# Optimization experiments

Measured on AMD Instinct MI355X. Metric: run time of the kernel, lower is better.

Reference implementation:

```python
import jax, jax.numpy as jnp
import numpy as np

B = 64            # number of graphs
NPG = 64          # nodes per graph (static; lengths are all equal here)
N = B * NPG       # total nodes = sum(lengths)
LT = 128          # max text tokens per node
LL = 32           # max labels per node
VOCAB = 50000
TOTAL_NUM = 100000
D = 256           # embedding_text == embedding_label == hidden_dimension
OUT = 1024


def setup_inputs() -> dict:
    key = jax.random.key(0)
    ks = jax.random.split(key, 12)
    return {
        "text_ids": jax.random.randint(ks[0], (N, LT), 0, VOCAB),
        "label_ids": jax.random.randint(ks[1], (N, LL), 0, TOTAL_NUM),
        "text_len": jax.random.randint(ks[2], (N,), 1, LT + 1),
        "label_len": jax.random.randint(ks[3], (N,), 1, LL + 1),
        "word_emb": jax.random.normal(ks[4], (VOCAB, D), jnp.float32) * 0.02,
        "label_emb": jax.random.normal(ks[5], (TOTAL_NUM, D), jnp.float32) * 0.02,
        "Wg_text": jax.random.normal(ks[6], (D, D), jnp.float32) * (1.0 / np.sqrt(D)),
        "Wg_label": jax.random.normal(ks[7], (D, D), jnp.float32) * (1.0 / np.sqrt(D)),
        "w_adap": jax.random.normal(ks[8], (2,), jnp.float32),
        "W1": jax.random.normal(ks[9], (D, D), jnp.float32) * (1.0 / np.sqrt(D)),
        "b1": jnp.zeros((D,), jnp.float32),
        "Wout": jax.random.normal(ks[10], (D, OUT), jnp.float32) * (1.0 / np.sqrt(D)),
        "bout": jnp.zeros((OUT,), jnp.float32),
    }


def _ragged_bag(table, ids, lens, mean):
    # gather rows then masked sum over the ragged axis (EmbeddingBag-style)
    L = ids.shape[1]
    mask = (jnp.arange(L)[None, :] < lens[:, None]).astype(table.dtype)  # [N, L]
    emb = table[ids]                                                     # [N, L, D]
    out = jnp.einsum("nld,nl->nd", emb, mask)
    if mean:
        out = out / lens[:, None].astype(table.dtype)
    return out


def reference(text_ids, label_ids, text_len, label_len, word_emb, label_emb,
              Wg_text, Wg_label, w_adap, W1, b1, Wout, bout):
    # fetchFeature: per-node ragged mean of word embeddings, ragged sum of label embeddings
    text_out = _ragged_bag(word_emb, text_ids, text_len, mean=True)    # [N, D]
    label_out = _ragged_bag(label_emb, label_ids, label_len, mean=False)  # [N, D]

    # weighted_GCN surrogate: per-type linear projection + relu, then per-graph mean readout
    h_t = jax.nn.relu(text_out @ Wg_text)   # [N, D]
    h_l = jax.nn.relu(label_out @ Wg_label)  # [N, D]
    seg = jnp.repeat(jnp.arange(B), NPG)     # graph id per node
    r_t = jax.ops.segment_sum(h_t, seg, num_segments=B) / NPG  # [B, D]
    r_l = jax.ops.segment_sum(h_l, seg, num_segments=B) / NPG  # [B, D]

    # adap: Linear(2,1,bias=False) over stacked (text,label), then MLLinear fusion
    fused = jnp.stack([r_t, r_l], axis=-1) @ w_adap  # [B, D]
    h = jax.nn.relu(fused @ W1 + b1)
    return h @ Wout + bout  # [B, OUT]
```

## Files before the change

### kernel.cpp

```cpp
#include <hip/hip_runtime.h>

#define NN      4096
#define BG      64
#define NPG_    64
#define LT_     128
#define LL_     32
#define D_      256
#define OUT_    1024

typedef __attribute__((ext_vector_type(8))) short bf16x8;
typedef __attribute__((ext_vector_type(4))) float f32x4;

__device__ __forceinline__ void split_bf16(float v, unsigned short& hi, unsigned short& lo) {
    union { float f; unsigned u; } a; a.f = v;
    const unsigned hu = (a.u + 0x8000u) & 0xFFFF0000u;
    union { unsigned u; float f; } h; h.u = hu;
    const float r = v - h.f;
    union { float f; unsigned u; } b; b.f = r;
    hi = (unsigned short)(hu >> 16);
    lo = (unsigned short)(((b.u + 0x8000u) & 0xFFFF0000u) >> 16);
}

__global__ __launch_bounds__(256) void convw_kernel(
    const float* __restrict__ Wg_text,
    const float* __restrict__ Wg_label,
    unsigned short* __restrict__ Wpk)
{
    const int b   = blockIdx.x;
    const int mat = b >> 7;
    const int nt  = (b >> 3) & 15;
    const int ks  = b & 7;
    const float* __restrict__ W = mat ? Wg_label : Wg_text;
    const int tid = threadIdx.x;

    #pragma unroll
    for (int r = 0; r < 2; ++r) {
        const int idx = tid + 256 * r;
        const int kl  = idx >> 4;
        const int c16 = idx & 15;
        const int k   = ks * 32 + kl;
        const float v = W[(size_t)k * D_ + nt * 16 + c16];
        unsigned short h, l;
        split_bf16(v, h, l);
        const int lane = c16 + 16 * ((kl >> 3) & 3);
        const int e    = kl & 7;
        const size_t bh = ((((size_t)mat * 2 + 0) * 16 + nt) * 8 + ks) * 512 + lane * 8 + e;
        const size_t bl = ((((size_t)mat * 2 + 1) * 16 + nt) * 8 + ks) * 512 + lane * 8 + e;
        Wpk[bh] = h;
        Wpk[bl] = l;
    }
}

__global__ __launch_bounds__(256) void gather_kernel(
    const int*   __restrict__ text_ids,
    const int*   __restrict__ label_ids,
    const int*   __restrict__ text_len,
    const int*   __restrict__ label_len,
    const float* __restrict__ word_emb,
    const float* __restrict__ label_emb,
    unsigned short* __restrict__ xh_t,
    unsigned short* __restrict__ xl_t,
    unsigned short* __restrict__ xh_l,
    unsigned short* __restrict__ xl_l)
{
    __shared__ int   sIds[LT_ + LL_];
    __shared__ float redT[4][D_];
    __shared__ float redL[4][D_];

    const int n    = blockIdx.x;
    const int tid  = threadIdx.x;
    const int wave = tid >> 6;
    const int lane = tid & 63;

    if (tid < LT_)               sIds[tid] = text_ids [(size_t)n * LT_ + tid];
    else if (tid < LT_ + LL_)    sIds[tid] = label_ids[(size_t)n * LL_ + (tid - LT_)];
    const int lt = text_len[n];
    const int ll = label_len[n];
    __syncthreads();

    float4 aT = make_float4(0.f, 0.f, 0.f, 0.f);
    float4 aL = make_float4(0.f, 0.f, 0.f, 0.f);

    {
        const float* __restrict__ bp = word_emb + (size_t)lane * 4;
        #pragma unroll 8
        for (int l = wave; l < lt; l += 4) {
            const float4 v = *reinterpret_cast<const float4*>(bp + (size_t)sIds[l] * D_);
            aT.x += v.x; aT.y += v.y; aT.z += v.z; aT.w += v.w;
        }
    }
    {
        const float* __restrict__ bp = label_emb + (size_t)lane * 4;
        #pragma unroll 8
        for (int l = wave; l < ll; l += 4) {
            const float4 v = *reinterpret_cast<const float4*>(bp + (size_t)sIds[LT_ + l] * D_);
            aL.x += v.x; aL.y += v.y; aL.z += v.z; aL.w += v.w;
        }
    }

    *reinterpret_cast<float4*>(&redT[wave][lane * 4]) = aT;
    *reinterpret_cast<float4*>(&redL[wave][lane * 4]) = aL;
    __syncthreads();

    const float t  = ((redT[0][tid] + redT[1][tid]) + (redT[2][tid] + redT[3][tid])) / (float)lt;
    const float lv =  (redL[0][tid] + redL[1][tid]) + (redL[2][tid] + redL[3][tid]);

    unsigned short h, l;
    const size_t o = (size_t)n * D_ + tid;
    split_bf16(t,  h, l);  xh_t[o] = h;  xl_t[o] = l;
    split_bf16(lv, h, l);  xh_l[o] = h;  xl_l[o] = l;
}

__global__ __launch_bounds__(512, 4) void proj_kernel(
    const unsigned short* __restrict__ xh_t,
    const unsigned short* __restrict__ xl_t,
    const unsigned short* __restrict__ xh_l,
    const unsigned short* __restrict__ xl_l,
    const unsigned short* __restrict__ Wpk,
    const float* __restrict__ w_adap,
    float*       __restrict__ h_comb)
{
    __shared__ __align__(16) short ldsX[4][16 * D_];

    const int tid   = threadIdx.x;
    const int wave  = tid >> 6;
    const int lane  = tid & 63;
    const int ntile = blockIdx.x >> 1;
    const int chalf = blockIdx.x & 1;
    const int base  = ntile * 16;

    {
        const int nd = tid >> 5, ch = tid & 31;
        const size_t g = (size_t)(base + nd) * D_ + ch * 8;
        const int d = nd * D_ + ((ch ^ (nd & 7)) * 8);
        *reinterpret_cast<int4*>(&ldsX[0][d]) = *reinterpret_cast<const int4*>(&xh_t[g]);
        *reinterpret_cast<int4*>(&ldsX[1][d]) = *reinterpret_cast<const int4*>(&xl_t[g]);
        *reinterpret_cast<int4*>(&ldsX[2][d]) = *reinterpret_cast<const int4*>(&xh_l[g]);
        *reinterpret_cast<int4*>(&ldsX[3][d]) = *reinterpret_cast<const int4*>(&xl_l[g]);
    }
    __syncthreads();

    const int nt  = chalf * 8 + wave;
    const int row = lane & 15;
    const int kc  = lane >> 4;
    f32x4 accT = {0.f, 0.f, 0.f, 0.f};
    f32x4 accL = {0.f, 0.f, 0.f, 0.f};

    #pragma unroll
    for (int ks = 0; ks < 8; ++ks) {
        const int aidx = row * D_ + (((ks * 4 + kc) ^ (row & 7)) * 8);
        const bf16x8 ath  = *reinterpret_cast<const bf16x8*>(&ldsX[0][aidx]);
        const bf16x8 atl  = *reinterpret_cast<const bf16x8*>(&ldsX[1][aidx]);
        const bf16x8 alh  = *reinterpret_cast<const bf16x8*>(&ldsX[2][aidx]);
        const bf16x8 all_ = *reinterpret_cast<const bf16x8*>(&ldsX[3][aidx]);

        const bf16x8 bth = *reinterpret_cast<const bf16x8*>(
            &Wpk[(((size_t)0 * 16 + nt) * 8 + ks) * 512 + lane * 8]);
        const bf16x8 btl = *reinterpret_cast<const bf16x8*>(
            &Wpk[(((size_t)1 * 16 + nt) * 8 + ks) * 512 + lane * 8]);
        const bf16x8 blh = *reinterpret_cast<const bf16x8*>(
            &Wpk[(((size_t)2 * 16 + nt) * 8 + ks) * 512 + lane * 8]);
        const bf16x8 bll = *reinterpret_cast<const bf16x8*>(
            &Wpk[(((size_t)3 * 16 + nt) * 8 + ks) * 512 + lane * 8]);

        accT = __builtin_amdgcn_mfma_f32_16x16x32_bf16(ath, bth, accT, 0, 0, 0);
        accT = __builtin_amdgcn_mfma_f32_16x16x32_bf16(ath, btl, accT, 0, 0, 0);
        accT = __builtin_amdgcn_mfma_f32_16x16x32_bf16(atl, bth, accT, 0, 0, 0);

        accL = __builtin_amdgcn_mfma_f32_16x16x32_bf16(alh, blh, accL, 0, 0, 0);
        accL = __builtin_amdgcn_mfma_f32_16x16x32_bf16(alh, bll, accL, 0, 0, 0);
        accL = __builtin_amdgcn_mfma_f32_16x16x32_bf16(all_, blh, accL, 0, 0, 0);
    }

    const float w0r = w_adap[0] * (1.0f / (float)NPG_);
    const float w1r = w_adap[1] * (1.0f / (float)NPG_);
    #pragma unroll
    for (int r = 0; r < 4; ++r) {
        const int node = base + kc * 4 + r;
        const int col  = nt * 16 + row;
        const float ht = accT[r] > 0.f ? accT[r] : 0.f;
        const float hl = accL[r] > 0.f ? accL[r] : 0.f;
        h_comb[(size_t)node * D_ + col] = w0r * ht + w1r * hl;
    }
}

__global__ __launch_bounds__(256) void graph_kernel(
    const float* __restrict__ h_comb,
    const float* __restrict__ W1,
    const float* __restrict__ b1,
    const float* __restrict__ Wout,
    const float* __restrict__ bout,
    float*       __restrict__ out)
{
    __shared__ float fused[D_];
    __shared__ float hrow[D_];

    const int bx   = blockIdx.x;
    const int b    = bx >> 2;
    const int part = bx & 3;
    const int tid  = threadIdx.x;

    float acc = 0.f;
    const float* __restrict__ basep = h_comb + (size_t)b * NPG_ * D_ + tid;
    #pragma unroll 8
    for (int n = 0; n < NPG_; ++n) acc += basep[(size_t)n * D_];
    fused[tid] = acc;
    __syncthreads();

    float a1 = b1[tid];
    for (int d = 0; d < D_; ++d)
        a1 = fmaf(fused[d], W1[(size_t)d * D_ + tid], a1);
    hrow[tid] = a1 > 0.f ? a1 : 0.f;
    __syncthreads();

    const int j = part * 256 + tid;
    float o = bout[j];
    for (int d = 0; d < D_; ++d)
        o = fmaf(hrow[d], Wout[(size_t)d * OUT_ + j], o);
    out[(size_t)b * OUT_ + j] = o;
}

extern "C" void kernel_launch(void* const* d_in, const int* in_sizes, int n_in,
                              void* d_out, int out_size, void* d_ws, size_t ws_size,
                              hipStream_t stream) {
    const int*   text_ids  = (const int*)  d_in[0];
    const int*   label_ids = (const int*)  d_in[1];
    const int*   text_len  = (const int*)  d_in[2];
    const int*   label_len = (const int*)  d_in[3];
    const float* word_emb  = (const float*)d_in[4];
    const float* label_emb = (const float*)d_in[5];
    const float* Wg_text   = (const float*)d_in[6];
    const float* Wg_label  = (const float*)d_in[7];
    const float* w_adap    = (const float*)d_in[8];
    const float* W1        = (const float*)d_in[9];
    const float* b1        = (const float*)d_in[10];
    const float* Wout      = (const float*)d_in[11];
    const float* bout      = (const float*)d_in[12];

    char* ws = (char*)d_ws;
    float*          h_comb = (float*)ws;
    unsigned short* xh_t   = (unsigned short*)(ws + (4  << 20));
    unsigned short* xl_t   = (unsigned short*)(ws + (6  << 20));
    unsigned short* xh_l   = (unsigned short*)(ws + (8  << 20));
    unsigned short* xl_l   = (unsigned short*)(ws + (10 << 20));
    unsigned short* Wpk    = (unsigned short*)(ws + (12 << 20));
    float*          out    = (float*)d_out;

    convw_kernel<<<256, 256, 0, stream>>>(Wg_text, Wg_label, Wpk);

    gather_kernel<<<NN, 256, 0, stream>>>(
        text_ids, label_ids, text_len, label_len,
        word_emb, label_emb, xh_t, xl_t, xh_l, xl_l);

    proj_kernel<<<NN / 16 * 2, 512, 0, stream>>>(
        xh_t, xl_t, xh_l, xl_l, Wpk, w_adap, h_comb);

    graph_kernel<<<BG * 4, 256, 0, stream>>>(
        h_comb, W1, b1, Wout, bout, out);
}
```

Before: 87.58 us.

## Fold weight conversion into gather kernel and pipeline projection operand loads

Result: faster. 84.70 us (-3.3%).

```diff
diff --git a/kernel.cpp b/kernel.cpp
--- a/kernel.cpp
+++ b/kernel.cpp
@@ -21,36 +21,6 @@
     lo = (unsigned short)(((b.u + 0x8000u) & 0xFFFF0000u) >> 16);
 }
 
-__global__ __launch_bounds__(256) void convw_kernel(
-    const float* __restrict__ Wg_text,
-    const float* __restrict__ Wg_label,
-    unsigned short* __restrict__ Wpk)
-{
-    const int b   = blockIdx.x;
-    const int mat = b >> 7;
-    const int nt  = (b >> 3) & 15;
-    const int ks  = b & 7;
-    const float* __restrict__ W = mat ? Wg_label : Wg_text;
-    const int tid = threadIdx.x;
-
-    #pragma unroll
-    for (int r = 0; r < 2; ++r) {
-        const int idx = tid + 256 * r;
-        const int kl  = idx >> 4;
-        const int c16 = idx & 15;
-        const int k   = ks * 32 + kl;
-        const float v = W[(size_t)k * D_ + nt * 16 + c16];
-        unsigned short h, l;
-        split_bf16(v, h, l);
-        const int lane = c16 + 16 * ((kl >> 3) & 3);
-        const int e    = kl & 7;
-        const size_t bh = ((((size_t)mat * 2 + 0) * 16 + nt) * 8 + ks) * 512 + lane * 8 + e;
-        const size_t bl = ((((size_t)mat * 2 + 1) * 16 + nt) * 8 + ks) * 512 + lane * 8 + e;
-        Wpk[bh] = h;
-        Wpk[bl] = l;
-    }
-}
-
 __global__ __launch_bounds__(256) void gather_kernel(
     const int*   __restrict__ text_ids,
     const int*   __restrict__ label_ids,
@@ -58,17 +28,45 @@
     const int*   __restrict__ label_len,
     const float* __restrict__ word_emb,
     const float* __restrict__ label_emb,
+    const float* __restrict__ Wg_text,
+    const float* __restrict__ Wg_label,
+    unsigned short* __restrict__ Wpk,
     unsigned short* __restrict__ xh_t,
     unsigned short* __restrict__ xl_t,
     unsigned short* __restrict__ xh_l,
     unsigned short* __restrict__ xl_l)
 {
+    const int tid  = threadIdx.x;
+
+    if (blockIdx.x >= NN) {
+        const int b   = blockIdx.x - NN;
+        const int mat = b >> 7;
+        const int nt  = (b >> 3) & 15;
+        const int ks  = b & 7;
+        const float* __restrict__ W = mat ? Wg_label : Wg_text;
+        #pragma unroll
+        for (int r = 0; r < 2; ++r) {
+            const int idx = tid + 256 * r;
+            const int kl  = idx >> 4;
+            const int c16 = idx & 15;
+            const int k   = ks * 32 + kl;
+            const float v = W[(size_t)k * D_ + nt * 16 + c16];
+            unsigned short h, l;
+            split_bf16(v, h, l);
+            const int lane = c16 + 16 * ((kl >> 3) & 3);
+            const int e    = kl & 7;
+            const size_t pb = (((size_t)nt * 8 + ks) * 4 + mat * 2) * 512 + lane * 8 + e;
+            Wpk[pb]       = h;
+            Wpk[pb + 512] = l;
+        }
+        return;
+    }
+
     __shared__ int   sIds[LT_ + LL_];
     __shared__ float redT[4][D_];
     __shared__ float redL[4][D_];
 
     const int n    = blockIdx.x;
-    const int tid  = threadIdx.x;
     const int wave = tid >> 6;
     const int lane = tid & 63;
 
@@ -111,7 +109,7 @@
     split_bf16(lv, h, l);  xh_l[o] = h;  xl_l[o] = l;
 }
 
-__global__ __launch_bounds__(512, 4) void proj_kernel(
+__global__ __launch_bounds__(256, 4) void proj_kernel(
     const unsigned short* __restrict__ xh_t,
     const unsigned short* __restrict__ xl_t,
     const unsigned short* __restrict__ xh_l,
@@ -125,12 +123,14 @@
     const int tid   = threadIdx.x;
     const int wave  = tid >> 6;
     const int lane  = tid & 63;
-    const int ntile = blockIdx.x >> 1;
-    const int chalf = blockIdx.x & 1;
+    const int ntile = blockIdx.x >> 2;
+    const int cq    = blockIdx.x & 3;
     const int base  = ntile * 16;
 
-    {
-        const int nd = tid >> 5, ch = tid & 31;
+    #pragma unroll
+    for (int r = 0; r < 2; ++r) {
+        const int idx = tid + 256 * r;
+        const int nd  = idx >> 5, ch = idx & 31;
         const size_t g = (size_t)(base + nd) * D_ + ch * 8;
         const int d = nd * D_ + ((ch ^ (nd & 7)) * 8);
         *reinterpret_cast<int4*>(&ldsX[0][d]) = *reinterpret_cast<const int4*>(&xh_t[g]);
@@ -140,36 +140,54 @@
     }
     __syncthreads();
 
-    const int nt  = chalf * 8 + wave;
+    const int nt  = cq * 4 + wave;
     const int row = lane & 15;
     const int kc  = lane >> 4;
+    const unsigned short* __restrict__ WpB = Wpk + ((size_t)nt * 8) * 4 * 512 + lane * 8;
+
     f32x4 accT = {0.f, 0.f, 0.f, 0.f};
     f32x4 accL = {0.f, 0.f, 0.f, 0.f};
 
+    bf16x8 cA0, cA1, cA2, cA3, cB0, cB1, cB2, cB3;
+    bf16x8 nA0, nA1, nA2, nA3, nB0, nB1, nB2, nB3;
+
+    {
+        const int aidx = row * D_ + ((kc ^ (row & 7)) * 8);
+        cA0 = *reinterpret_cast<const bf16x8*>(&ldsX[0][aidx]);
+        cA1 = *reinterpret_cast<const bf16x8*>(&ldsX[1][aidx]);
+        cA2 = *reinterpret_cast<const bf16x8*>(&ldsX[2][aidx]);
+        cA3 = *reinterpret_cast<const bf16x8*>(&ldsX[3][aidx]);
+        const unsigned short* p = WpB;
+        cB0 = *reinterpret_cast<const bf16x8*>(p);
+        cB1 = *reinterpret_cast<const bf16x8*>(p + 512);
+        cB2 = *reinterpret_cast<const bf16x8*>(p + 1024);
+        cB3 = *reinterpret_cast<const bf16x8*>(p + 1536);
+    }
+
     #pragma unroll
     for (int ks = 0; ks < 8; ++ks) {
-        const int aidx = row * D_ + (((ks * 4 + kc) ^ (row & 7)) * 8);
-        const bf16x8 ath  = *reinterpret_cast<const bf16x8*>(&ldsX[0][aidx]);
-        const bf16x8 atl  = *reinterpret_cast<const bf16x8*>(&ldsX[1][aidx]);
-        const bf16x8 alh  = *reinterpret_cast<const bf16x8*>(&ldsX[2][aidx]);
-        const bf16x8 all_ = *reinterpret_cast<const bf16x8*>(&ldsX[3][aidx]);
-
-        const bf16x8 bth = *reinterpret_cast<const bf16x8*>(
-            &Wpk[(((size_t)0 * 16 + nt) * 8 + ks) * 512 + lane * 8]);
-        const bf16x8 btl = *reinterpret_cast<const bf16x8*>(
-            &Wpk[(((size_t)1 * 16 + nt) * 8 + ks) * 512 + lane * 8]);
-        const bf16x8 blh = *reinterpret_cast<const bf16x8*>(
-            &Wpk[(((size_t)2 * 16 + nt) * 8 + ks) * 512 + lane * 8]);
-        const bf16x8 bll = *reinterpret_cast<const bf16x8*>(
-            &Wpk[(((size_t)3 * 16 + nt) * 8 + ks) * 512 + lane * 8]);
-
-        accT = __builtin_amdgcn_mfma_f32_16x16x32_bf16(ath, bth, accT, 0, 0, 0);
-        accT = __builtin_amdgcn_mfma_f32_16x16x32_bf16(ath, btl, accT, 0, 0, 0);
-        accT = __builtin_amdgcn_mfma_f32_16x16x32_bf16(atl, bth, accT, 0, 0, 0);
-
-        accL = __builtin_amdgcn_mfma_f32_16x16x32_bf16(alh, blh, accL, 0, 0, 0);
-        accL = __builtin_amdgcn_mfma_f32_16x16x32_bf16(alh, bll, accL, 0, 0, 0);
-        accL = __builtin_amdgcn_mfma_f32_16x16x32_bf16(all_, blh, accL, 0, 0, 0);
+        if (ks < 7) {
+            const int aidx = row * D_ + ((((ks + 1) * 4 + kc) ^ (row & 7)) * 8);
+            nA0 = *reinterpret_cast<const bf16x8*>(&ldsX[0][aidx]);
+            nA1 = *reinterpret_cast<const bf16x8*>(&ldsX[1][aidx]);
+            nA2 = *reinterpret_cast<const bf16x8*>(&ldsX[2][aidx]);
+            nA3 = *reinterpret_cast<const bf16x8*>(&ldsX[3][aidx]);
+            const unsigned short* p = WpB + (size_t)(ks + 1) * 2048;
+            nB0 = *reinterpret_cast<const bf16x8*>(p);
+            nB1 = *reinterpret_cast<const bf16x8*>(p + 512);
+            nB2 = *reinterpret_cast<const bf16x8*>(p + 1024);
+            nB3 = *reinterpret_cast<const bf16x8*>(p + 1536);
+        }
+
+        accT = __builtin_amdgcn_mfma_f32_16x16x32_bf16(cA0, cB0, accT, 0, 0, 0);
+        accT = __builtin_amdgcn_mfma_f32_16x16x32_bf16(cA0, cB1, accT, 0, 0, 0);
+        accT = __builtin_amdgcn_mfma_f32_16x16x32_bf16(cA1, cB0, accT, 0, 0, 0);
+        accL = __builtin_amdgcn_mfma_f32_16x16x32_bf16(cA2, cB2, accL, 0, 0, 0);
+        accL = __builtin_amdgcn_mfma_f32_16x16x32_bf16(cA2, cB3, accL, 0, 0, 0);
+        accL = __builtin_amdgcn_mfma_f32_16x16x32_bf16(cA3, cB2, accL, 0, 0, 0);
+
+        cA0 = nA0; cA1 = nA1; cA2 = nA2; cA3 = nA3;
+        cB0 = nB0; cB1 = nB1; cB2 = nB2; cB3 = nB3;
     }
 
     const float w0r = w_adap[0] * (1.0f / (float)NPG_);
@@ -207,17 +225,32 @@
     fused[tid] = acc;
     __syncthreads();
 
-    float a1 = b1[tid];
-    for (int d = 0; d < D_; ++d)
-        a1 = fmaf(fused[d], W1[(size_t)d * D_ + tid], a1);
-    hrow[tid] = a1 > 0.f ? a1 : 0.f;
+    {
+        float s0 = 0.f, s1 = 0.f, s2 = 0.f, s3 = 0.f;
+        const float* __restrict__ wp = W1 + tid;
+        for (int d = 0; d < D_; d += 4) {
+            s0 = fmaf(fused[d + 0], wp[(size_t)(d + 0) * D_], s0);
+            s1 = fmaf(fused[d + 1], wp[(size_t)(d + 1) * D_], s1);
+            s2 = fmaf(fused[d + 2], wp[(size_t)(d + 2) * D_], s2);
+            s3 = fmaf(fused[d + 3], wp[(size_t)(d + 3) * D_], s3);
+        }
+        const float a1 = b1[tid] + ((s0 + s1) + (s2 + s3));
+        hrow[tid] = a1 > 0.f ? a1 : 0.f;
+    }
     __syncthreads();
 
     const int j = part * 256 + tid;
-    float o = bout[j];
-    for (int d = 0; d < D_; ++d)
-        o = fmaf(hrow[d], Wout[(size_t)d * OUT_ + j], o);
-    out[(size_t)b * OUT_ + j] = o;
+    {
+        float s0 = 0.f, s1 = 0.f, s2 = 0.f, s3 = 0.f;
+        const float* __restrict__ wp = Wout + j;
+        for (int d = 0; d < D_; d += 4) {
+            s0 = fmaf(hrow[d + 0], wp[(size_t)(d + 0) * OUT_], s0);
+            s1 = fmaf(hrow[d + 1], wp[(size_t)(d + 1) * OUT_], s1);
+            s2 = fmaf(hrow[d + 2], wp[(size_t)(d + 2) * OUT_], s2);
+            s3 = fmaf(hrow[d + 3], wp[(size_t)(d + 3) * OUT_], s3);
+        }
+        out[(size_t)b * OUT_ + j] = bout[j] + ((s0 + s1) + (s2 + s3));
+    }
 }
 
 extern "C" void kernel_launch(void* const* d_in, const int* in_sizes, int n_in,
@@ -246,13 +279,12 @@
     unsigned short* Wpk    = (unsigned short*)(ws + (12 << 20));
     float*          out    = (float*)d_out;
 
-    convw_kernel<<<256, 256, 0, stream>>>(Wg_text, Wg_label, Wpk);
-
-    gather_kernel<<<NN, 256, 0, stream>>>(
+    gather_kernel<<<NN + 256, 256, 0, stream>>>(
         text_ids, label_ids, text_len, label_len,
-        word_emb, label_emb, xh_t, xl_t, xh_l, xl_l);
-
-    proj_kernel<<<NN / 16 * 2, 512, 0, stream>>>(
+        word_emb, label_emb, Wg_text, Wg_label, Wpk,
+        xh_t, xl_t, xh_l, xl_l);
+
+    proj_kernel<<<NN / 16 * 4, 256, 0, stream>>>(
         xh_t, xl_t, xh_l, xl_l, Wpk, w_adap, h_comb);
 
     graph_kernel<<<BG * 4, 256, 0, stream>>>(
```
